# Kernel optimization log

Hardware: AMD Instinct MI355X
Metric: run time of the kernel (lower is better)

## Reference

```python
import jax, jax.numpy as jnp
import numpy as np

B, S, D, H, F = 8, 1024, 1024, 16, 4096
DH = D // H  # 64
EPS = 1e-12


def _layer_norm(x, g, b):
    mu = jnp.mean(x, axis=-1, keepdims=True)
    var = jnp.mean(jnp.square(x - mu), axis=-1, keepdims=True)
    return (x - mu) / jnp.sqrt(var + EPS) * g + b


def setup_inputs() -> dict:
    key = jax.random.key(0)
    ks = jax.random.split(key, 16)
    sd = 0.02
    inp = {
        "x": jax.random.normal(ks[0], (B, S, D), dtype=jnp.float32),
        "attn_mask": jnp.ones((B, S), dtype=jnp.int32),
        # attention projections (torch Linear: W is [out, in])
        "Wq": jax.random.normal(ks[1], (D, D), dtype=jnp.float32) * sd,
        "bq": jnp.zeros((D,), dtype=jnp.float32),
        "Wk": jax.random.normal(ks[2], (D, D), dtype=jnp.float32) * sd,
        "bk": jnp.zeros((D,), dtype=jnp.float32),
        "Wv": jax.random.normal(ks[3], (D, D), dtype=jnp.float32) * sd,
        "bv": jnp.zeros((D,), dtype=jnp.float32),
        "Wo": jax.random.normal(ks[4], (D, D), dtype=jnp.float32) * sd,
        "bo": jnp.zeros((D,), dtype=jnp.float32),
        # sa_layer_norm
        "ln1_g": jnp.ones((D,), dtype=jnp.float32),
        "ln1_b": jnp.zeros((D,), dtype=jnp.float32),
        # FFN
        "W1": jax.random.normal(ks[5], (F, D), dtype=jnp.float32) * sd,
        "b1": jnp.zeros((F,), dtype=jnp.float32),
        "W2": jax.random.normal(ks[6], (D, F), dtype=jnp.float32) * sd,
        "b2": jnp.zeros((D,), dtype=jnp.float32),
        # output_layer_norm
        "ln2_g": jnp.ones((D,), dtype=jnp.float32),
        "ln2_b": jnp.zeros((D,), dtype=jnp.float32),
    }
    return inp


def reference(x, attn_mask, Wq, bq, Wk, bk, Wv, bv, Wo, bo,
              ln1_g, ln1_b, W1, b1, W2, b2, ln2_g, ln2_b):
    b, s, d = x.shape

    def proj_heads(inp, W, bias):
        y = jnp.einsum('bsd,ed->bse', inp, W) + bias  # torch Linear: x @ W.T + b
        return y.reshape(b, s, H, DH).transpose(0, 2, 1, 3)  # (b, h, s, dh)

    q = proj_heads(x, Wq, bq) / jnp.sqrt(jnp.float32(DH))
    k = proj_heads(x, Wk, bk)
    v = proj_heads(x, Wv, bv)

    scores = jnp.einsum('bhqe,bhke->bhqk', q, k)  # (b, h, s, s)
    pad = (attn_mask == 0)[:, None, None, :]      # (b, 1, 1, s)
    scores = jnp.where(pad, -jnp.inf, scores)
    weights = jax.nn.softmax(scores, axis=-1)

    ctx = jnp.einsum('bhqk,bhke->bhqe', weights, v)
    ctx = ctx.transpose(0, 2, 1, 3).reshape(b, s, d)
    sa_out = jnp.einsum('bsd,ed->bse', ctx, Wo) + bo

    h = _layer_norm(sa_out + x, ln1_g, ln1_b)

    ff = jnp.einsum('bsd,fd->bsf', h, W1) + b1
    ff = jax.nn.gelu(ff, approximate=False)
    ff = jnp.einsum('bsf,df->bsd', ff, W2) + b2

    out = _layer_norm(ff + h, ln2_g, ln2_b)
    return out
```

## Files before the change

### kernel.cpp

```cpp
#include <hip/hip_runtime.h>
#include <math.h>

typedef __attribute__((ext_vector_type(8))) short short8;
typedef __attribute__((ext_vector_type(4))) float f32x4;

__device__ __forceinline__ unsigned short f2bf(float f) {
  unsigned int u = __float_as_uint(f);
  u += 0x7fffu + ((u >> 16) & 1u);
  return (unsigned short)(u >> 16);
}

__device__ __forceinline__ float gelu_f(float v) {
  float xa = fabsf(v) * 0.70710678118f;
  float t = __builtin_amdgcn_rcpf(1.f + 0.3275911f * xa);
  float p = t * (0.254829592f +
            t * (-0.284496736f +
            t * (1.421413741f +
            t * (-1.453152027f + t * 1.061405429f))));
  float erfa = 1.f - p * __expf(-xa * xa);
  return 0.5f * v * (1.f + copysignf(erfa, v));
}

__device__ __forceinline__ void gll16(const unsigned short* g, unsigned short* l) {
  __builtin_amdgcn_global_load_lds(
      (const __attribute__((address_space(1))) unsigned int*)(uintptr_t)g,
      (__attribute__((address_space(3))) unsigned int*)(uintptr_t)l, 16, 0, 0);
}

__global__ __launch_bounds__(256) void cvt_all(
    const float* __restrict__ Wq, const float* __restrict__ Wk,
    const float* __restrict__ Wv, const float* __restrict__ Wo,
    const float* __restrict__ W1, const float* __restrict__ W2,
    const float* __restrict__ x, unsigned short* __restrict__ ws) {
  const int bi = blockIdx.x;
  const float* in;
  unsigned short* out;
  int i;
  if (bi < 4096) {
    const int m = bi >> 10;
    in = (m == 0) ? Wq : (m == 1) ? Wk : (m == 2) ? Wv : Wo;
    out = ws + (size_t)m * (1u << 20);
    i = (bi & 1023) * 256 + threadIdx.x;
  } else if (bi < 8192) {
    in = W1; out = ws + (4u << 20); i = (bi - 4096) * 256 + threadIdx.x;
  } else if (bi < 12288) {
    in = W2; out = ws + (8u << 20); i = (bi - 8192) * 256 + threadIdx.x;
  } else {
    in = x; out = ws + (12u << 20); i = (bi - 12288) * 256 + threadIdx.x;
  }
  float4 f = reinterpret_cast<const float4*>(in)[i];
  ushort4 o;
  o.x = f2bf(f.x); o.y = f2bf(f.y); o.z = f2bf(f.z); o.w = f2bf(f.w);
  reinterpret_cast<ushort4*>(out)[i] = o;
}

#define MFMA_SUB(f0, SA)                                                      \
  {                                                                           \
    __builtin_amdgcn_s_setprio(1);                                            \
    _Pragma("unroll") for (int fi = 0; fi < 2; ++fi) {                        \
      _Pragma("unroll") for (int j = 0; j < NREP; ++j) {                      \
        if constexpr (SWAP) {                                                 \
          acc[(f0) + fi][j] = __builtin_amdgcn_mfma_f32_16x16x32_bf16(        \
              bf[j][0], SA[fi][0], acc[(f0) + fi][j], 0, 0, 0);               \
        } else {                                                              \
          acc[(f0) + fi][j] = __builtin_amdgcn_mfma_f32_16x16x32_bf16(        \
              SA[fi][0], bf[j][0], acc[(f0) + fi][j], 0, 0, 0);               \
        }                                                                     \
      }                                                                       \
    }                                                                         \
    _Pragma("unroll") for (int fi = 0; fi < 2; ++fi) {                        \
      _Pragma("unroll") for (int j = 0; j < NREP; ++j) {                      \
        if constexpr (SWAP) {                                                 \
          acc[(f0) + fi][j] = __builtin_amdgcn_mfma_f32_16x16x32_bf16(        \
              bf[j][1], SA[fi][1], acc[(f0) + fi][j], 0, 0, 0);               \
        } else {                                                              \
          acc[(f0) + fi][j] = __builtin_amdgcn_mfma_f32_16x16x32_bf16(        \
              SA[fi][1], bf[j][1], acc[(f0) + fi][j], 0, 0, 0);               \
        }                                                                     \
      }                                                                       \
    }                                                                         \
    __builtin_amdgcn_s_setprio(0);                                            \
  }

#define READ_AF(SET, f0)                                                      \
  {                                                                           \
    SET[0][0] = *reinterpret_cast<const short8*>(                             \
        &Asc[abase + ((f0) * 16) * 64 + s0]);                                 \
    SET[0][1] = *reinterpret_cast<const short8*>(                             \
        &Asc[abase + ((f0) * 16) * 64 + s1]);                                 \
    SET[1][0] = *reinterpret_cast<const short8*>(                             \
        &Asc[abase + ((f0) * 16 + 16) * 64 + s0]);                            \
    SET[1][1] = *reinterpret_cast<const short8*>(                             \
        &Asc[abase + ((f0) * 16 + 16) * 64 + s1]);                            \
  }

#define READ_BF                                                               \
  _Pragma("unroll") for (int j = 0; j < NREP; ++j) {                          \
    bf[j][0] = *reinterpret_cast<const short8*>(                              \
        &Bsc[bbase + (j * 16) * 64 + s0]);                                    \
    bf[j][1] = *reinterpret_cast<const short8*>(                              \
        &Bsc[bbase + (j * 16) * 64 + s1]);                                    \
  }

#define LGKM(n)                                                               \
  asm volatile("s_waitcnt lgkmcnt(" #n ")" ::: "memory");                     \
  __builtin_amdgcn_sched_barrier(0)

#define MEMFENCE asm volatile("" ::: "memory")
#define BAR __builtin_amdgcn_s_barrier()

template <int EPI, int BN, bool SWAP>
__global__ __launch_bounds__(512, 2) void gemm_big(
    const unsigned short* __restrict__ A, const unsigned short* __restrict__ B,
    const float* __restrict__ bias, const float* __restrict__ bias_k,
    int K, int N, const float* __restrict__ resid,
    unsigned short* __restrict__ outb, float* __restrict__ outf) {
  constexpr int WN = BN / 4;
  constexpr int NREP = WN / 16;
  constexpr int BGRP = BN / 64;
  __shared__ __align__(16) unsigned short As[2][256 * 64];
  __shared__ __align__(16) unsigned short Bs[2][BN * 64];

  const int t = threadIdx.x;
  const int lane = t & 63, wv = t >> 6;
  const int wm = wv >> 2, wn = wv & 3;
  const int l15 = lane & 15, quad = lane >> 4;

  const int gx = gridDim.x;
  const int nwg = gx * gridDim.y;
  int lin = blockIdx.y * gx + blockIdx.x;
  lin = (lin & 7) * (nwg >> 3) + (lin >> 3);
  const int gxs = 31 - __clz(gx);
  const int tn = (lin & (gx - 1)) * BN;
  const int tm = (lin >> gxs) * 256;

  const int srow = lane >> 3;
  const int scol = ((lane & 7) ^ srow) << 3;
  const unsigned short* pA[4];
  const unsigned short* pB[BGRP];
#pragma unroll
  for (int g = 0; g < 4; ++g)
    pA[g] = &A[(size_t)(tm + g * 64 + wv * 8 + srow) * K + scol];
#pragma unroll
  for (int g = 0; g < BGRP; ++g)
    pB[g] = &B[(size_t)(tn + g * 64 + wv * 8 + srow) * K + scol];

  const int abase = (wm * 128 + l15) * 64;
  const int bbase = (wn * WN + l15) * 64;
  const int s0 = ((quad ^ (l15 & 7)) << 3);
  const int s1 = (((quad + 4) ^ (l15 & 7)) << 3);

  const f32x4 zero = {0.f, 0.f, 0.f, 0.f};
  f32x4 acc[8][NREP];
#pragma unroll
  for (int i = 0; i < 8; ++i)
#pragma unroll
    for (int j = 0; j < NREP; ++j) acc[i][j] = zero;
  short8 afA[2][2], afB[2][2], bf[NREP][2];

#pragma unroll
  for (int g = 0; g < 4; ++g) {
    gll16(pA[g], &As[0][(g * 64 + wv * 8) * 64]);
    pA[g] += 64;
  }
#pragma unroll
  for (int g = 0; g < BGRP; ++g) {
    gll16(pB[g], &Bs[0][(g * 64 + wv * 8) * 64]);
    pB[g] += 64;
  }
  asm volatile("s_waitcnt vmcnt(0)" ::: "memory");
  BAR;
  MEMFENCE;

  const int NT = K >> 6;
  for (int tt = 0; tt < NT; ++tt) {
    const unsigned short* Asc = As[tt & 1];
    const unsigned short* Bsc = Bs[tt & 1];
    unsigned short* Asn = As[(tt + 1) & 1];
    unsigned short* Bsn = Bs[(tt + 1) & 1];

    if (tt + 1 < NT) {
#pragma unroll
      for (int g = 0; g < 4; ++g) {
        gll16(pA[g], &Asn[(g * 64 + wv * 8) * 64]);
        pA[g] += 64;
      }
#pragma unroll
      for (int g = 0; g < BGRP; ++g) {
        gll16(pB[g], &Bsn[(g * 64 + wv * 8) * 64]);
        pB[g] += 64;
      }
    }

    READ_BF;
    READ_AF(afA, 0);
    READ_AF(afB, 2);
    LGKM(4);
    MFMA_SUB(0, afA);
    READ_AF(afA, 4);
    LGKM(4);
    MFMA_SUB(2, afB);
    READ_AF(afB, 6);
    LGKM(4);
    MFMA_SUB(4, afA);
    LGKM(0);
    MFMA_SUB(6, afB);

    if (tt + 1 < NT) {
      asm volatile("s_waitcnt vmcnt(0)" ::: "memory");
      BAR;
      MEMFENCE;
    }
  }

  if constexpr (!SWAP) {
    const int rb2 = tm + wm * 128 + (quad << 2);
    const int cb2 = tn + wn * WN + l15;
#pragma unroll
    for (int i = 0; i < 8; ++i) {
      const int row0 = rb2 + i * 16;
#pragma unroll
      for (int j = 0; j < NREP; ++j) {
        const int col = cb2 + j * 16;
        const float bcol = bias[col];
        const int h = col >> 6, dh = col & 63;
        const int b = row0 >> 10, s0r = row0 & 1023;
        ushort4 pk;
        pk.x = f2bf(acc[i][j][0] + bcol);
        pk.y = f2bf(acc[i][j][1] + bcol);
        pk.z = f2bf(acc[i][j][2] + bcol);
        pk.w = f2bf(acc[i][j][3] + bcol);
        *reinterpret_cast<ushort4*>(
            &outb[(((size_t)((b << 4) + h)) << 16) + (dh << 10) + s0r]) = pk;
      }
    }
  } else {
    const int rb = tm + wm * 128 + l15;
    const int cb = tn + wn * WN + (quad << 2);
#pragma unroll
    for (int i = 0; i < 8; ++i) {
      const int row = rb + i * 16;
#pragma unroll
      for (int j = 0; j < NREP; ++j) {
        const int col0 = cb + j * 16;
        if constexpr (EPI == 5) {
          const int chunk = col0 >> 10;
          const int colc = col0 & 1023;
          const float4 b4 = *reinterpret_cast<const float4*>(
              &(chunk == 0 ? bias : bias_k)[colc]);
          const float sc = (chunk == 0) ? 0.125f : 1.f;
          const int h = colc >> 6, dh = colc & 63;
          const int b = row >> 10, s = row & 1023;
          ushort4 pk;
          pk.x = f2bf((acc[i][j][0] + b4.x) * sc);
          pk.y = f2bf((acc[i][j][1] + b4.y) * sc);
          pk.z = f2bf((acc[i][j][2] + b4.z) * sc);
          pk.w = f2bf((acc[i][j][3] + b4.w) * sc);
          *reinterpret_cast<ushort4*>(
              &outb[((size_t)chunk << 23) + (((size_t)((b << 4) + h)) << 16) +
                    (s << 6) + dh]) = pk;
        } else if constexpr (EPI == 2) {
          const float4 b4 = *reinterpret_cast<const float4*>(&bias[col0]);
          ushort4 pk;
          pk.x = f2bf(gelu_f(acc[i][j][0] + b4.x));
          pk.y = f2bf(gelu_f(acc[i][j][1] + b4.y));
          pk.z = f2bf(gelu_f(acc[i][j][2] + b4.z));
          pk.w = f2bf(gelu_f(acc[i][j][3] + b4.w));
          *reinterpret_cast<ushort4*>(&outb[(size_t)row * (size_t)N + col0]) = pk;
        } else {
          const float4 b4 = *reinterpret_cast<const float4*>(&bias[col0]);
          const size_t idx = (size_t)row * (size_t)N + col0;
          const float4 r4 = *reinterpret_cast<const float4*>(&resid[idx]);
          float4 o4;
          o4.x = acc[i][j][0] + b4.x + r4.x;
          o4.y = acc[i][j][1] + b4.y + r4.y;
          o4.z = acc[i][j][2] + b4.z + r4.z;
          o4.w = acc[i][j][3] + b4.w + r4.w;
          *reinterpret_cast<float4*>(&outf[idx]) = o4;
        }
      }
    }
  }
}
#undef MFMA_SUB
#undef READ_AF
#undef READ_BF
#undef LGKM
#undef MEMFENCE
#undef BAR

__global__ __launch_bounds__(256) void attn_kernel(
    const unsigned short* __restrict__ Q, const unsigned short* __restrict__ Kc,
    const unsigned short* __restrict__ Vg, const int* __restrict__ mask,
    unsigned short* __restrict__ ctx) {
  __shared__ __align__(16) unsigned short Ks[2][64 * 64];
  __shared__ __align__(16) unsigned short Vs[2][64 * 64];
  __shared__ __align__(16) unsigned short Ps[4][16 * 72];
  __shared__ float maskf[1024];
  const int t = threadIdx.x;
  const int bh = blockIdx.x;
  const int qt = blockIdx.y;
  const int b = bh >> 4, h = bh & 15;
  const int lane = t & 63, wv = t >> 6, l15 = lane & 15, quad = lane >> 4;
  const int lr = lane >> 3;
  const int cs = (lane & 7) ^ lr;
  const unsigned short* Qp = Q + ((size_t)bh << 16);
  const unsigned short* Kp = Kc + ((size_t)bh << 16);
  const unsigned short* Vp = Vg + ((size_t)bh << 16);
  const int seg0 = wv * 2, seg1 = wv * 2 + 1;
  const int r0 = seg0 * 8 + lr, r1 = seg1 * 8 + lr;

  for (int i = t; i < 1024; i += 256)
    maskf[i] = mask[b * 1024 + i] ? -8.f : -INFINITY;

  short8 qf[2][2];
#pragma unroll
  for (int g = 0; g < 2; ++g)
#pragma unroll
    for (int hh = 0; hh < 2; ++hh)
      qf[g][hh] = *reinterpret_cast<const short8*>(
          &Qp[(size_t)(qt * 128 + wv * 32 + g * 16 + l15) * 64 + hh * 32 + quad * 8]);

  gll16(&Kp[r0 * 64 + cs * 8], &Ks[0][seg0 * 512]);
  gll16(&Kp[r1 * 64 + cs * 8], &Ks[0][seg1 * 512]);
  gll16(&Vp[r0 * 1024 + cs * 8], &Vs[0][seg0 * 512]);
  gll16(&Vp[r1 * 1024 + cs * 8], &Vs[0][seg1 * 512]);

  const int sw0 = ((quad ^ (l15 & 7)) << 3);
  const int sw1 = (((quad + 4) ^ (l15 & 7)) << 3);
  const f32x4 zero = {0.f, 0.f, 0.f, 0.f};
  float ps[2][4];
  f32x4 o[2][4];
#pragma unroll
  for (int g = 0; g < 2; ++g)
#pragma unroll
    for (int j = 0; j < 4; ++j) { o[g][j] = zero; ps[g][j] = 0.f; }

  unsigned short* Pw = Ps[wv];
  for (int kt = 0; kt < 16; ++kt) {
    __syncthreads();
    const int cur = kt & 1;
    if (kt < 15) {
      const int nb = cur ^ 1;
      gll16(&Kp[((kt + 1) * 64 + r0) * 64 + cs * 8], &Ks[nb][seg0 * 512]);
      gll16(&Kp[((kt + 1) * 64 + r1) * 64 + cs * 8], &Ks[nb][seg1 * 512]);
      gll16(&Vp[r0 * 1024 + (kt + 1) * 64 + cs * 8], &Vs[nb][seg0 * 512]);
      gll16(&Vp[r1 * 1024 + (kt + 1) * 64 + cs * 8], &Vs[nb][seg1 * 512]);
    }
    float madd[4];
    short8 kf[4][2];
#pragma unroll
    for (int nt = 0; nt < 4; ++nt) {
      const int row = (nt * 16 + l15) * 64;
      kf[nt][0] = *reinterpret_cast<const short8*>(&Ks[cur][row + sw0]);
      kf[nt][1] = *reinterpret_cast<const short8*>(&Ks[cur][row + sw1]);
      madd[nt] = maskf[kt * 64 + nt * 16 + l15];
    }
#pragma unroll
    for (int g = 0; g < 2; ++g) {
      f32x4 s4[4];
#pragma unroll
      for (int nt = 0; nt < 4; ++nt) {
        s4[nt] = __builtin_amdgcn_mfma_f32_16x16x32_bf16(qf[g][0], kf[nt][0], zero, 0, 0, 0);
        s4[nt] = __builtin_amdgcn_mfma_f32_16x16x32_bf16(qf[g][1], kf[nt][1], s4[nt], 0, 0, 0);
      }
#pragma unroll
      for (int nt = 0; nt < 4; ++nt) {
#pragma unroll
        for (int r = 0; r < 4; ++r) {
          float p = __expf(s4[nt][r] + madd[nt]);
          ps[g][r] += p;
          Pw[(quad * 4 + r) * 72 + nt * 16 + l15] = f2bf(p);
        }
      }
      short8 pf0 = *reinterpret_cast<const short8*>(&Pw[l15 * 72 + quad * 8]);
      short8 pf1 = *reinterpret_cast<const short8*>(&Pw[l15 * 72 + 32 + quad * 8]);
#pragma unroll
      for (int nt = 0; nt < 4; ++nt) {
        const int row = (nt * 16 + l15) * 64;
        short8 vf0 = *reinterpret_cast<const short8*>(&Vs[cur][row + sw0]);
        short8 vf1 = *reinterpret_cast<const short8*>(&Vs[cur][row + sw1]);
        o[g][nt] = __builtin_amdgcn_mfma_f32_16x16x32_bf16(pf0, vf0, o[g][nt], 0, 0, 0);
        o[g][nt] = __builtin_amdgcn_mfma_f32_16x16x32_bf16(pf1, vf1, o[g][nt], 0, 0, 0);
      }
    }
  }

#pragma unroll
  for (int g = 0; g < 2; ++g)
#pragma unroll
    for (int r = 0; r < 4; ++r) {
      float v = ps[g][r];
#pragma unroll
      for (int off = 8; off >= 1; off >>= 1) v += __shfl_xor(v, off, 64);
      const float inv = 1.f / v;
      const int srow = qt * 128 + wv * 32 + g * 16 + quad * 4 + r;
#pragma unroll
      for (int nt = 0; nt < 4; ++nt) {
        const int dh = nt * 16 + l15;
        ctx[((size_t)b << 20) + ((size_t)srow << 10) + (h << 6) + dh] =
            f2bf(o[g][nt][r] * inv);
      }
    }
}

__global__ __launch_bounds__(256) void ln_kernel(float* __restrict__ y,
                                                 const float* __restrict__ g,
                                                 const float* __restrict__ be,
                                                 unsigned short* __restrict__ hb) {
  __shared__ float sm[8];
  const int t = threadIdx.x;
  const size_t row = blockIdx.x;
  float* yr = y + (row << 10);
  const float4 v = reinterpret_cast<const float4*>(yr)[t];
  float s = v.x + v.y + v.z + v.w;
#pragma unroll
  for (int off = 32; off >= 1; off >>= 1) s += __shfl_xor(s, off, 64);
  if ((t & 63) == 0) sm[t >> 6] = s;
  __syncthreads();
  float mu = (sm[0] + sm[1] + sm[2] + sm[3]) * (1.f / 1024.f);
  const float dx = v.x - mu, dy = v.y - mu, dz = v.z - mu, dw = v.w - mu;
  float q = dx * dx + dy * dy + dz * dz + dw * dw;
#pragma unroll
  for (int off = 32; off >= 1; off >>= 1) q += __shfl_xor(q, off, 64);
  if ((t & 63) == 0) sm[4 + (t >> 6)] = q;
  __syncthreads();
  float var = (sm[4] + sm[5] + sm[6] + sm[7]) * (1.f / 1024.f);
  float rs = rsqrtf(var + 1e-12f);
  const float4 g4 = reinterpret_cast<const float4*>(g)[t];
  const float4 b4 = reinterpret_cast<const float4*>(be)[t];
  float4 o4;
  o4.x = dx * rs * g4.x + b4.x;
  o4.y = dy * rs * g4.y + b4.y;
  o4.z = dz * rs * g4.z + b4.z;
  o4.w = dw * rs * g4.w + b4.w;
  reinterpret_cast<float4*>(yr)[t] = o4;
  if (hb) {
    ushort4 pk;
    pk.x = f2bf(o4.x); pk.y = f2bf(o4.y); pk.z = f2bf(o4.z); pk.w = f2bf(o4.w);
    reinterpret_cast<ushort4*>(hb + (row << 10))[t] = pk;
  }
}

extern "C" void kernel_launch(void* const* d_in, const int* in_sizes, int n_in,
                              void* d_out, int out_size, void* d_ws, size_t ws_size,
                              hipStream_t stream) {
  const float* x   = (const float*)d_in[0];
  const int*   msk = (const int*)d_in[1];
  const float* Wq  = (const float*)d_in[2];
  const float* bq  = (const float*)d_in[3];
  const float* Wk  = (const float*)d_in[4];
  const float* bk  = (const float*)d_in[5];
  const float* Wv  = (const float*)d_in[6];
  const float* bv  = (const float*)d_in[7];
  const float* Wo  = (const float*)d_in[8];
  const float* bo  = (const float*)d_in[9];
  const float* g1  = (const float*)d_in[10];
  const float* be1 = (const float*)d_in[11];
  const float* W1  = (const float*)d_in[12];
  const float* b1  = (const float*)d_in[13];
  const float* W2  = (const float*)d_in[14];
  const float* b2  = (const float*)d_in[15];
  const float* g2  = (const float*)d_in[16];
  const float* be2 = (const float*)d_in[17];
  float* out = (float*)d_out;

  unsigned short* Wqb = (unsigned short*)d_ws;
  unsigned short* Wvb = Wqb + (2u << 20);
  unsigned short* Wob = Wvb + (1u << 20);
  unsigned short* W1b = Wob + (1u << 20);
  unsigned short* W2b = W1b + (4u << 20);
  unsigned short* xb  = W2b + (4u << 20);
  unsigned short* qb  = xb + (8u << 20);
  unsigned short* vb  = qb + (16u << 20);
  unsigned short* ctx = xb;
  unsigned short* ffb = xb;
  float* y1 = (float*)(qb + (24u << 20));
  unsigned short* hb = (unsigned short*)(y1 + (8u << 20));

  dim3 blk(256), blk5(512);
  cvt_all<<<dim3(20480), blk, 0, stream>>>(Wq, Wk, Wv, Wo, W1, W2, x, (unsigned short*)d_ws);
  gemm_big<5, 256, true><<<dim3(8, 32), blk5, 0, stream>>>(xb, Wqb, bq, bk, 1024, 2048,
                                                           nullptr, qb, nullptr);
  gemm_big<4, 128, false><<<dim3(8, 32), blk5, 0, stream>>>(xb, Wvb, bv, nullptr, 1024, 1024,
                                                            nullptr, vb, nullptr);
  attn_kernel<<<dim3(128, 8), blk, 0, stream>>>(qb, qb + (8u << 20), vb, msk, ctx);
  gemm_big<1, 128, true><<<dim3(8, 32), blk5, 0, stream>>>(ctx, Wob, bo, nullptr, 1024, 1024,
                                                           x, nullptr, y1);
  ln_kernel<<<dim3(8192), blk, 0, stream>>>(y1, g1, be1, hb);
  gemm_big<2, 256, true><<<dim3(16, 32), blk5, 0, stream>>>(hb, W1b, b1, nullptr, 1024, 4096,
                                                            nullptr, ffb, nullptr);
  gemm_big<1, 128, true><<<dim3(8, 32), blk5, 0, stream>>>(ffb, W2b, b2, nullptr, 4096, 1024,
                                                           y1, nullptr, out);
  ln_kernel<<<dim3(8192), blk, 0, stream>>>(out, g2, be2, nullptr);
}
```

Before: 481.8 us.

## Load V fragments directly from global memory and drop LDS mask staging

The attention kernel no longer stages V tiles and the mask in shared memory. V fragments are read straight from global memory into registers each key tile, split so the second half loads after the QK MFMAs. The mask is read from global memory per tile instead of a precomputed LDS array, and launch bounds now request 4 blocks per CU. This cuts LDS footprint and LDS traffic so more blocks can be resident, but each V read becomes an uncoalesced global load with no double-buffered prefetch, which risks latency stalls.

```diff
diff --git a/kernel.cpp b/kernel.cpp
--- a/kernel.cpp
+++ b/kernel.cpp
@@ -289,14 +289,12 @@
 #undef MEMFENCE
 #undef BAR
 
-__global__ __launch_bounds__(256) void attn_kernel(
+__global__ __launch_bounds__(256, 4) void attn_kernel(
     const unsigned short* __restrict__ Q, const unsigned short* __restrict__ Kc,
     const unsigned short* __restrict__ Vg, const int* __restrict__ mask,
     unsigned short* __restrict__ ctx) {
   __shared__ __align__(16) unsigned short Ks[2][64 * 64];
-  __shared__ __align__(16) unsigned short Vs[2][64 * 64];
   __shared__ __align__(16) unsigned short Ps[4][16 * 72];
-  __shared__ float maskf[1024];
   const int t = threadIdx.x;
   const int bh = blockIdx.x;
   const int qt = blockIdx.y;
@@ -307,11 +305,9 @@
   const unsigned short* Qp = Q + ((size_t)bh << 16);
   const unsigned short* Kp = Kc + ((size_t)bh << 16);
   const unsigned short* Vp = Vg + ((size_t)bh << 16);
+  const int* mb = mask + b * 1024;
   const int seg0 = wv * 2, seg1 = wv * 2 + 1;
   const int r0 = seg0 * 8 + lr, r1 = seg1 * 8 + lr;
-
-  for (int i = t; i < 1024; i += 256)
-    maskf[i] = mask[b * 1024 + i] ? -8.f : -INFINITY;
 
   short8 qf[2][2];
 #pragma unroll
@@ -323,8 +319,6 @@
 
   gll16(&Kp[r0 * 64 + cs * 8], &Ks[0][seg0 * 512]);
   gll16(&Kp[r1 * 64 + cs * 8], &Ks[0][seg1 * 512]);
-  gll16(&Vp[r0 * 1024 + cs * 8], &Vs[0][seg0 * 512]);
-  gll16(&Vp[r1 * 1024 + cs * 8], &Vs[0][seg1 * 512]);
 
   const int sw0 = ((quad ^ (l15 & 7)) << 3);
   const int sw1 = (((quad + 4) ^ (l15 & 7)) << 3);
@@ -344,8 +338,6 @@
       const int nb = cur ^ 1;
       gll16(&Kp[((kt + 1) * 64 + r0) * 64 + cs * 8], &Ks[nb][seg0 * 512]);
       gll16(&Kp[((kt + 1) * 64 + r1) * 64 + cs * 8], &Ks[nb][seg1 * 512]);
-      gll16(&Vp[r0 * 1024 + (kt + 1) * 64 + cs * 8], &Vs[nb][seg0 * 512]);
-      gll16(&Vp[r1 * 1024 + (kt + 1) * 64 + cs * 8], &Vs[nb][seg1 * 512]);
     }
     float madd[4];
     short8 kf[4][2];
@@ -354,8 +346,13 @@
       const int row = (nt * 16 + l15) * 64;
       kf[nt][0] = *reinterpret_cast<const short8*>(&Ks[cur][row + sw0]);
       kf[nt][1] = *reinterpret_cast<const short8*>(&Ks[cur][row + sw1]);
-      madd[nt] = maskf[kt * 64 + nt * 16 + l15];
-    }
+      madd[nt] = mb[kt * 64 + nt * 16 + l15] ? -8.f : -INFINITY;
+    }
+    short8 vf0[4], vf1[4];
+#pragma unroll
+    for (int nt = 0; nt < 4; ++nt)
+      vf0[nt] = *reinterpret_cast<const short8*>(
+          &Vp[(size_t)(nt * 16 + l15) * 1024 + kt * 64 + quad * 8]);
 #pragma unroll
     for (int g = 0; g < 2; ++g) {
       f32x4 s4[4];
@@ -363,6 +360,12 @@
       for (int nt = 0; nt < 4; ++nt) {
         s4[nt] = __builtin_amdgcn_mfma_f32_16x16x32_bf16(qf[g][0], kf[nt][0], zero, 0, 0, 0);
         s4[nt] = __builtin_amdgcn_mfma_f32_16x16x32_bf16(qf[g][1], kf[nt][1], s4[nt], 0, 0, 0);
+      }
+      if (g == 0) {
+#pragma unroll
+        for (int nt = 0; nt < 4; ++nt)
+          vf1[nt] = *reinterpret_cast<const short8*>(
+              &Vp[(size_t)(nt * 16 + l15) * 1024 + kt * 64 + 32 + quad * 8]);
       }
 #pragma unroll
       for (int nt = 0; nt < 4; ++nt) {
@@ -377,11 +380,8 @@
       short8 pf1 = *reinterpret_cast<const short8*>(&Pw[l15 * 72 + 32 + quad * 8]);
 #pragma unroll
       for (int nt = 0; nt < 4; ++nt) {
-        const int row = (nt * 16 + l15) * 64;
-        short8 vf0 = *reinterpret_cast<const short8*>(&Vs[cur][row + sw0]);
-        short8 vf1 = *reinterpret_cast<const short8*>(&Vs[cur][row + sw1]);
-        o[g][nt] = __builtin_amdgcn_mfma_f32_16x16x32_bf16(pf0, vf0, o[g][nt], 0, 0, 0);
-        o[g][nt] = __builtin_amdgcn_mfma_f32_16x16x32_bf16(pf1, vf1, o[g][nt], 0, 0, 0);
+        o[g][nt] = __builtin_amdgcn_mfma_f32_16x16x32_bf16(pf0, vf0[nt], o[g][nt], 0, 0, 0);
+        o[g][nt] = __builtin_amdgcn_mfma_f32_16x16x32_bf16(pf1, vf1[nt], o[g][nt], 0, 0, 0);
       }
     }
   }
```

New measurement: 532.1 us. 1.1x slower.
